# Kernel tuning notes

Hardware: AMD Instinct MI355X
Metric: run time of the kernel (lower is better)

Reference implementation:

```python
import jax, jax.numpy as jnp
import numpy as np


def _cxcywh_to_xyxy(b):
    cx, cy, w, h = b[..., 0], b[..., 1], b[..., 2], b[..., 3]
    return jnp.stack([cx - 0.5 * w, cy - 0.5 * h, cx + 0.5 * w, cy + 0.5 * h], axis=-1)


def _generalized_box_iou(a, b):
    # a: [M,4] xyxy, b: [N,4] xyxy -> [M,N] GIoU matrix (DETR box_ops semantics)
    area_a = (a[:, 2] - a[:, 0]) * (a[:, 3] - a[:, 1])  # [M]
    area_b = (b[:, 2] - b[:, 0]) * (b[:, 3] - b[:, 1])  # [N]
    lt = jnp.maximum(a[:, None, :2], b[None, :, :2])    # [M,N,2]
    rb = jnp.minimum(a[:, None, 2:], b[None, :, 2:])
    wh = jnp.clip(rb - lt, 0.0)
    inter = wh[..., 0] * wh[..., 1]                     # [M,N]
    union = area_a[:, None] + area_b[None, :] - inter
    iou = inter / union
    lt_c = jnp.minimum(a[:, None, :2], b[None, :, :2])
    rb_c = jnp.maximum(a[:, None, 2:], b[None, :, 2:])
    wh_c = jnp.clip(rb_c - lt_c, 0.0)
    area_c = wh_c[..., 0] * wh_c[..., 1]
    return iou - (area_c - union) / area_c


def setup_inputs() -> dict:
    key = jax.random.key(0)
    k1, k2, k3 = jax.random.split(key, 3)
    B, T, N = 8, 64, 8
    # predicted boxes in cxcywh, all components in (0,1) -> positive w,h (valid)
    pred_boxes = jax.random.uniform(k1, (B, T, N, 4), dtype=jnp.float32)
    # target boxes directly in valid xyxy (code path uses them unconverted)
    centers = jax.random.uniform(k2, (B, T, N, 2), dtype=jnp.float32) * 0.8 + 0.1
    half_wh = (jax.random.uniform(k3, (B, T, N, 2), dtype=jnp.float32) * 0.2 + 0.02) * 0.5
    bboxes = jnp.concatenate([centers - half_wh, centers + half_wh], axis=-1)
    bboxes_mask = jnp.ones((B, T), dtype=bool)
    return {"pred_boxes": pred_boxes, "bboxes": bboxes, "bboxes_mask": bboxes_mask}


def reference(pred_boxes, bboxes, bboxes_mask):
    B, T, N, _ = pred_boxes.shape
    M = B * T * N
    # per-box validity (mask is per-frame, broadcast to boxes), as weights
    v = jnp.broadcast_to(bboxes_mask[:, :, None], (B, T, N)).reshape(M).astype(pred_boxes.dtype)
    src = _cxcywh_to_xyxy(pred_boxes.reshape(M, 4))   # [M,4]
    tgt = bboxes.reshape(M, 4)                        # [M,4]
    G = _generalized_box_iou(tgt, src)                # [M,M] rows=targets, cols=preds
    # argmax matching over valid prediction columns
    g_match = jnp.where(v[None, :] > 0, G, -jnp.inf)
    idx = jnp.argmax(g_match, axis=1)                 # [M]
    matched = src[idx]                                # [M,4]
    matched_gious = G[:, idx]                         # [M,M] (faithful to original)
    w = v[:, None] * v[idx][None, :]                  # validity weights
    loss_giou = 1.0 - jnp.sum(matched_gious * w) / jnp.sum(w)
    loss_bbox = jnp.sum(jnp.abs(matched - tgt) * v[:, None]) / (4.0 * jnp.sum(v))
    return loss_giou, loss_bbox
```

## Files before the change

### kernel.cpp

```cpp
#include <hip/hip_runtime.h>
#include <cmath>

#define WAVE 64
#define TPB  256
#define FTPB 1024
#define KEY_INIT 0x007FFFFFFFFFFFFFull

__device__ __forceinline__ float fastrcp(float x) { return __builtin_amdgcn_rcpf(x); }

__device__ __forceinline__ unsigned sortable_u32(float f) {
    unsigned b = __float_as_uint(f);
    return (b & 0x80000000u) ? ~b : (b | 0x80000000u);
}

__device__ __forceinline__ int mask_mode(const void* maskp) {
    const unsigned char* mb = (const unsigned char*)maskp;
    unsigned char b0 = mb[0], b1 = mb[1];
    if (b0 != 0 && b1 != 0) return 0;
    if (b0 != 0) return 1;
    return 2;
}
__device__ __forceinline__ float mask_v(const void* maskp, int t, int mode) {
    if (mode == 0) return ((const unsigned char*)maskp)[t] ? 1.0f : 0.0f;
    if (mode == 1) return ((const int*)maskp)[t] ? 1.0f : 0.0f;
    return (((const float*)maskp)[t] != 0.0f) ? 1.0f : 0.0f;
}
__device__ __forceinline__ int midx(int m, int nsh, int N) {
    return (nsh >= 0) ? (m >> nsh) : (m / N);
}

__global__ __launch_bounds__(TPB) void prep_kernel(
        const float4* __restrict__ pred, const float4* __restrict__ tgt,
        const void* __restrict__ maskp, int M, int nsh, int N,
        float4* __restrict__ convS, float* __restrict__ areaS,
        float* __restrict__ areaT, float* __restrict__ vv,
        unsigned long long* __restrict__ rowkey, float* __restrict__ colsumG) {
    int m = blockIdx.x * blockDim.x + threadIdx.x;
    if (m >= M) return;
    float4 p = pred[m];
    float x1 = p.x - 0.5f * p.z, y1 = p.y - 0.5f * p.w;
    float x2 = p.x + 0.5f * p.z, y2 = p.y + 0.5f * p.w;
    convS[m] = make_float4(x1, y1, x2, y2);
    areaS[m] = (x2 - x1) * (y2 - y1);
    float4 t = tgt[m];
    areaT[m] = (t.z - t.x) * (t.w - t.y);
    vv[m] = mask_v(maskp, midx(m, nsh, N), mask_mode(maskp));
    rowkey[m] = KEY_INIT;
    colsumG[m] = 0.0f;
}

__global__ __launch_bounds__(TPB) void pass_kernel(
        const float4* __restrict__ tgt, const float* __restrict__ areaT,
        const float4* __restrict__ convS, const float* __restrict__ areaS,
        const float* __restrict__ vv, int M,
        unsigned long long* __restrict__ rowkey, float* __restrict__ colsumG) {
    const int CC   = M >> 6;
    const int wid  = blockIdx.x * (TPB / WAVE) + (threadIdx.x >> 6);
    const int lane = threadIdx.x & (WAVE - 1);
    const int rb   = wid / CC;
    const int cc   = wid % CC;
    const int r    = rb * 64 + lane;
    const int c0   = cc * 64;

    float4 a  = tgt[r];
    float  aA = areaT[r];
    float  vi = vv[r];

    float vc = vv[c0 + lane];
    unsigned long long cm = __ballot(vc > 0.0f);

    float best = -INFINITY;
    int   bidx = 0;
    float csum = 0.0f;

    const float4* __restrict__ bcol = convS + c0;
    const float*  __restrict__ bare = areaS + c0;

#pragma unroll 8
    for (int j = 0; j < 64; ++j) {
        float4 b  = bcol[j];
        float  aB = bare[j];
        float ltx = fmaxf(a.x, b.x), lty = fmaxf(a.y, b.y);
        float rbx = fminf(a.z, b.z), rby = fminf(a.w, b.w);
        float w = fmaxf(rbx - ltx, 0.0f), h = fmaxf(rby - lty, 0.0f);
        float inter = w * h;
        float uni = aA + aB - inter;
        float cx1 = fminf(a.x, b.x), cy1 = fminf(a.y, b.y);
        float cx2 = fmaxf(a.z, b.z), cy2 = fmaxf(a.w, b.w);
        float areaC = (cx2 - cx1) * (cy2 - cy1);
        float hval = fmaf(uni, fastrcp(areaC), inter * fastrcp(uni));

        float t = vi * hval;
        for (int off = 1; off <= 32; off <<= 1) t += __shfl_xor(t, off);
        csum = (lane == j) ? t : csum;

        if ((cm >> j) & 1ull) {
            if (hval > best) { best = hval; bidx = c0 + j; }
        }
    }

    unsigned long long key = ((unsigned long long)sortable_u32(best) << 32)
                           | (unsigned)(~bidx);
    atomicMax(&rowkey[r], key);
    atomicAdd(&colsumG[c0 + lane], csum);
}

__device__ __forceinline__ double wave_sum_d(double x) {
    for (int off = 32; off >= 1; off >>= 1) x += __shfl_xor(x, off);
    return x;
}

__global__ __launch_bounds__(FTPB) void finalize_kernel(
        const float4* __restrict__ convS, const float4* __restrict__ tgt,
        const float* __restrict__ vv, const unsigned long long* __restrict__ rowkey,
        const float* __restrict__ colsumG, int M, float* __restrict__ out) {
    __shared__ double red[4 * (FTPB / WAVE)];
    const int tid = threadIdx.x;

    double sumV = 0.0, S2 = 0.0, S1h = 0.0, bbox = 0.0;
    for (int m = tid; m < M; m += FTPB) {
        float vi = vv[m];
        int   k  = (int)(~(unsigned)rowkey[m]);
        float vk = vv[k];
        sumV += (double)vi;
        S2   += (double)vk;
        S1h  += (double)vk * (double)colsumG[k];
        float4 s = convS[k];
        float4 t = tgt[m];
        bbox += (double)vi * (double)(fabsf(s.x - t.x) + fabsf(s.y - t.y) +
                                      fabsf(s.z - t.z) + fabsf(s.w - t.w));
    }
    sumV = wave_sum_d(sumV);
    S2   = wave_sum_d(S2);
    S1h  = wave_sum_d(S1h);
    bbox = wave_sum_d(bbox);
    int wid = tid >> 6, lane = tid & (WAVE - 1);
    const int NW = FTPB / WAVE;
    if (lane == 0) {
        red[wid] = sumV; red[NW + wid] = S2; red[2 * NW + wid] = S1h; red[3 * NW + wid] = bbox;
    }
    __syncthreads();
    if (tid == 0) {
        double a = 0, b = 0, c = 0, d = 0;
        for (int w = 0; w < NW; ++w) {
            a += red[w]; b += red[NW + w]; c += red[2 * NW + w]; d += red[3 * NW + w];
        }
        out[0] = (float)(2.0 - c / (a * b));
        out[1] = (float)(d / (4.0 * a));
    }
}

extern "C" void kernel_launch(void* const* d_in, const int* in_sizes, int n_in,
                              void* d_out, int out_size, void* d_ws, size_t ws_size,
                              hipStream_t stream) {
    const float4* pred = (const float4*)d_in[0];
    const float4* tgt  = (const float4*)d_in[1];
    const void*   mask = d_in[2];

    int M = in_sizes[0] / 4;
    int N = M / in_sizes[2];
    int nsh = -1;
    for (int s = 0; s < 31; ++s) if ((1 << s) == N) { nsh = s; break; }

    char* ws = (char*)d_ws;
    float4* convS   = (float4*)ws;             ws += (size_t)M * 16;
    float*  areaS   = (float*)ws;              ws += (size_t)M * 4;
    float*  areaT   = (float*)ws;              ws += (size_t)M * 4;
    float*  vv      = (float*)ws;              ws += (size_t)M * 4;
    unsigned long long* rowkey = (unsigned long long*)ws; ws += (size_t)M * 8;
    float*  colsumG = (float*)ws;              ws += (size_t)M * 4;
    float*  out = (float*)d_out;

    prep_kernel<<<(M + TPB - 1) / TPB, TPB, 0, stream>>>(
        pred, tgt, mask, M, nsh, N, convS, areaS, areaT, vv, rowkey, colsumG);

    int waves  = (M / 64) * (M / 64);
    int blocks = waves / (TPB / WAVE);
    pass_kernel<<<blocks, TPB, 0, stream>>>(
        tgt, areaT, convS, areaS, vv, M, rowkey, colsumG);

    finalize_kernel<<<1, FTPB, 0, stream>>>(convS, tgt, vv, rowkey, colsumG, M, out);
}
```

Before: 95.53 us.

## Split row-argmax and column-sum into separate passes with partial buffers instead of atomics

Replaces the single pass that did per-iteration wave shuffles for column sums plus atomics with two block groups. One computes the per-row argmax keys and the other the per-column GIoU sums, and both write partial results to C×M buffers. A new reduce kernel combines these partials, and prep now precomputes 64-bit validity masks per chunk. This removes the shuffle reductions and atomics at the cost of computing every GIoU twice, an extra launch, and several MB of partial-buffer traffic.

```diff
diff --git a/kernel.cpp b/kernel.cpp
--- a/kernel.cpp
+++ b/kernel.cpp
@@ -4,7 +4,6 @@
 #define WAVE 64
 #define TPB  256
 #define FTPB 1024
-#define KEY_INIT 0x007FFFFFFFFFFFFFull
 
 __device__ __forceinline__ float fastrcp(float x) { return __builtin_amdgcn_rcpf(x); }
 
@@ -34,7 +33,7 @@
         const void* __restrict__ maskp, int M, int nsh, int N,
         float4* __restrict__ convS, float* __restrict__ areaS,
         float* __restrict__ areaT, float* __restrict__ vv,
-        unsigned long long* __restrict__ rowkey, float* __restrict__ colsumG) {
+        unsigned long long* __restrict__ cmask) {
     int m = blockIdx.x * blockDim.x + threadIdx.x;
     if (m >= M) return;
     float4 p = pred[m];
@@ -44,65 +43,98 @@
     areaS[m] = (x2 - x1) * (y2 - y1);
     float4 t = tgt[m];
     areaT[m] = (t.z - t.x) * (t.w - t.y);
-    vv[m] = mask_v(maskp, midx(m, nsh, N), mask_mode(maskp));
-    rowkey[m] = KEY_INIT;
-    colsumG[m] = 0.0f;
+    float vm = mask_v(maskp, midx(m, nsh, N), mask_mode(maskp));
+    vv[m] = vm;
+    unsigned long long bal = __ballot(vm > 0.0f);
+    if ((threadIdx.x & (WAVE - 1)) == 0) cmask[m >> 6] = bal;
 }
 
 __global__ __launch_bounds__(TPB) void pass_kernel(
         const float4* __restrict__ tgt, const float* __restrict__ areaT,
         const float4* __restrict__ convS, const float* __restrict__ areaS,
-        const float* __restrict__ vv, int M,
-        unsigned long long* __restrict__ rowkey, float* __restrict__ colsumG) {
-    const int CC   = M >> 6;
-    const int wid  = blockIdx.x * (TPB / WAVE) + (threadIdx.x >> 6);
-    const int lane = threadIdx.x & (WAVE - 1);
-    const int rb   = wid / CC;
-    const int cc   = wid % CC;
-    const int r    = rb * 64 + lane;
-    const int c0   = cc * 64;
-
-    float4 a  = tgt[r];
-    float  aA = areaT[r];
-    float  vi = vv[r];
-
-    float vc = vv[c0 + lane];
-    unsigned long long cm = __ballot(vc > 0.0f);
-
-    float best = -INFINITY;
-    int   bidx = 0;
-    float csum = 0.0f;
-
-    const float4* __restrict__ bcol = convS + c0;
-    const float*  __restrict__ bare = areaS + c0;
-
+        const unsigned long long* __restrict__ cmask, int M, int rowBlocks,
+        unsigned long long* __restrict__ keypart, float* __restrict__ colpart) {
+    const int C   = M >> 6;
+    const int tid = threadIdx.x;
+
+    if ((int)blockIdx.x < rowBlocks) {
+        const int rb = blockIdx.x / C;
+        const int cc = blockIdx.x % C;
+        const int r  = rb * TPB + tid;
+        float4 a  = tgt[r];
+        float  aA = areaT[r];
+        const unsigned long long cm = cmask[cc];
+        const float4* __restrict__ bc = convS + (size_t)cc * 64;
+        const float*  __restrict__ ba = areaS + (size_t)cc * 64;
+
+        float best = -INFINITY;
+        int   bidx = 0;
 #pragma unroll 8
-    for (int j = 0; j < 64; ++j) {
-        float4 b  = bcol[j];
-        float  aB = bare[j];
-        float ltx = fmaxf(a.x, b.x), lty = fmaxf(a.y, b.y);
-        float rbx = fminf(a.z, b.z), rby = fminf(a.w, b.w);
-        float w = fmaxf(rbx - ltx, 0.0f), h = fmaxf(rby - lty, 0.0f);
-        float inter = w * h;
-        float uni = aA + aB - inter;
-        float cx1 = fminf(a.x, b.x), cy1 = fminf(a.y, b.y);
-        float cx2 = fmaxf(a.z, b.z), cy2 = fmaxf(a.w, b.w);
-        float areaC = (cx2 - cx1) * (cy2 - cy1);
-        float hval = fmaf(uni, fastrcp(areaC), inter * fastrcp(uni));
-
-        float t = vi * hval;
-        for (int off = 1; off <= 32; off <<= 1) t += __shfl_xor(t, off);
-        csum = (lane == j) ? t : csum;
-
-        if ((cm >> j) & 1ull) {
-            if (hval > best) { best = hval; bidx = c0 + j; }
+        for (int j = 0; j < 64; ++j) {
+            if (!((cm >> j) & 1ull)) continue;
+            float4 b  = bc[j];
+            float  aB = ba[j];
+            float ltx = fmaxf(a.x, b.x), lty = fmaxf(a.y, b.y);
+            float rbx = fminf(a.z, b.z), rby = fminf(a.w, b.w);
+            float w = fmaxf(rbx - ltx, 0.0f), h = fmaxf(rby - lty, 0.0f);
+            float inter = w * h;
+            float uni = aA + aB - inter;
+            float cx1 = fminf(a.x, b.x), cy1 = fminf(a.y, b.y);
+            float cx2 = fmaxf(a.z, b.z), cy2 = fmaxf(a.w, b.w);
+            float areaC = (cx2 - cx1) * (cy2 - cy1);
+            float hval = fmaf(uni, fastrcp(areaC), inter * fastrcp(uni));
+            if (hval > best) { best = hval; bidx = cc * 64 + j; }
         }
-    }
-
-    unsigned long long key = ((unsigned long long)sortable_u32(best) << 32)
-                           | (unsigned)(~bidx);
-    atomicMax(&rowkey[r], key);
-    atomicAdd(&colsumG[c0 + lane], csum);
+        unsigned long long key = ((unsigned long long)sortable_u32(best) << 32)
+                               | (unsigned)(~bidx);
+        keypart[(size_t)cc * M + r] = key;
+    } else {
+        const int bb2 = blockIdx.x - rowBlocks;
+        const int cb = bb2 / C;
+        const int rc = bb2 % C;
+        const int c  = cb * TPB + tid;
+        float4 b  = convS[c];
+        float  aB = areaS[c];
+        const unsigned long long rm = cmask[rc];
+        const float4* __restrict__ ar  = tgt   + (size_t)rc * 64;
+        const float*  __restrict__ aar = areaT + (size_t)rc * 64;
+
+        float csum = 0.0f;
+#pragma unroll 8
+        for (int j = 0; j < 64; ++j) {
+            if (!((rm >> j) & 1ull)) continue;
+            float4 a  = ar[j];
+            float  aA = aar[j];
+            float ltx = fmaxf(a.x, b.x), lty = fmaxf(a.y, b.y);
+            float rbx = fminf(a.z, b.z), rby = fminf(a.w, b.w);
+            float w = fmaxf(rbx - ltx, 0.0f), h = fmaxf(rby - lty, 0.0f);
+            float inter = w * h;
+            float uni = aA + aB - inter;
+            float cx1 = fminf(a.x, b.x), cy1 = fminf(a.y, b.y);
+            float cx2 = fmaxf(a.z, b.z), cy2 = fmaxf(a.w, b.w);
+            float areaC = (cx2 - cx1) * (cy2 - cy1);
+            float hval = fmaf(uni, fastrcp(areaC), inter * fastrcp(uni));
+            csum += hval;
+        }
+        colpart[(size_t)rc * M + c] = csum;
+    }
+}
+
+__global__ __launch_bounds__(TPB) void reduce_kernel(
+        const unsigned long long* __restrict__ keypart,
+        const float* __restrict__ colpart, int M, int C,
+        int* __restrict__ idx, float* __restrict__ colsumh) {
+    int m = blockIdx.x * blockDim.x + threadIdx.x;
+    if (m >= M) return;
+    unsigned long long k = keypart[m];
+    float s = colpart[m];
+    for (int cc = 1; cc < C; ++cc) {
+        unsigned long long kc = keypart[(size_t)cc * M + m];
+        k = (kc > k) ? kc : k;
+        s += colpart[(size_t)cc * M + m];
+    }
+    idx[m] = (int)(~(unsigned)k);
+    colsumh[m] = s;
 }
 
 __device__ __forceinline__ double wave_sum_d(double x) {
@@ -112,19 +144,19 @@
 
 __global__ __launch_bounds__(FTPB) void finalize_kernel(
         const float4* __restrict__ convS, const float4* __restrict__ tgt,
-        const float* __restrict__ vv, const unsigned long long* __restrict__ rowkey,
-        const float* __restrict__ colsumG, int M, float* __restrict__ out) {
+        const float* __restrict__ vv, const int* __restrict__ idx,
+        const float* __restrict__ colsumh, int M, float* __restrict__ out) {
     __shared__ double red[4 * (FTPB / WAVE)];
     const int tid = threadIdx.x;
 
     double sumV = 0.0, S2 = 0.0, S1h = 0.0, bbox = 0.0;
     for (int m = tid; m < M; m += FTPB) {
         float vi = vv[m];
-        int   k  = (int)(~(unsigned)rowkey[m]);
+        int   k  = idx[m];
         float vk = vv[k];
         sumV += (double)vi;
         S2   += (double)vk;
-        S1h  += (double)vk * (double)colsumG[k];
+        S1h  += (double)vk * (double)colsumh[k];
         float4 s = convS[k];
         float4 t = tgt[m];
         bbox += (double)vi * (double)(fabsf(s.x - t.x) + fabsf(s.y - t.y) +
@@ -162,22 +194,30 @@
     int nsh = -1;
     for (int s = 0; s < 31; ++s) if ((1 << s) == N) { nsh = s; break; }
 
+    int C = M >> 6;
+
     char* ws = (char*)d_ws;
     float4* convS   = (float4*)ws;             ws += (size_t)M * 16;
     float*  areaS   = (float*)ws;              ws += (size_t)M * 4;
     float*  areaT   = (float*)ws;              ws += (size_t)M * 4;
     float*  vv      = (float*)ws;              ws += (size_t)M * 4;
-    unsigned long long* rowkey = (unsigned long long*)ws; ws += (size_t)M * 8;
-    float*  colsumG = (float*)ws;              ws += (size_t)M * 4;
+    unsigned long long* cmaskp = (unsigned long long*)ws; ws += (size_t)C * 8;
+    unsigned long long* keypart = (unsigned long long*)ws; ws += (size_t)C * M * 8;
+    float*  colpart = (float*)ws;              ws += (size_t)C * M * 4;
+    int*    idx     = (int*)ws;                ws += (size_t)M * 4;
+    float*  colsumh = (float*)ws;              ws += (size_t)M * 4;
     float*  out = (float*)d_out;
 
     prep_kernel<<<(M + TPB - 1) / TPB, TPB, 0, stream>>>(
-        pred, tgt, mask, M, nsh, N, convS, areaS, areaT, vv, rowkey, colsumG);
-
-    int waves  = (M / 64) * (M / 64);
-    int blocks = waves / (TPB / WAVE);
-    pass_kernel<<<blocks, TPB, 0, stream>>>(
-        tgt, areaT, convS, areaS, vv, M, rowkey, colsumG);
-
-    finalize_kernel<<<1, FTPB, 0, stream>>>(convS, tgt, vv, rowkey, colsumG, M, out);
-}
+        pred, tgt, mask, M, nsh, N, convS, areaS, areaT, vv, cmaskp);
+
+    int rowBlocks = (M / TPB) * C;
+    int colBlocks = rowBlocks;
+    pass_kernel<<<rowBlocks + colBlocks, TPB, 0, stream>>>(
+        tgt, areaT, convS, areaS, cmaskp, M, rowBlocks, keypart, colpart);
+
+    reduce_kernel<<<(M + TPB - 1) / TPB, TPB, 0, stream>>>(
+        keypart, colpart, M, C, idx, colsumh);
+
+    finalize_kernel<<<1, FTPB, 0, stream>>>(convS, tgt, vv, idx, colsumh, M, out);
+}
```

Result: slower. 114.3 us (+19.6%).

## Fuse prep, pairwise pass and finalize into one kernel with split row/column blocks

Applied to the files above, without the earlier changes.

Replaces the three-kernel pipeline with one kernel. Half of the blocks compute per-row argmax partial keys and the other half compute per-column GIoU partial sums; both recompute box conversion and areas on the fly. The last block, found through an atomic counter, reduces the partials and computes the losses. This removes the per-iteration wave shuffle reduction, the global atomics and the extra launches, at the cost of evaluating the pairwise GIoU twice and a serial single-block partial reduction.

```diff
diff --git a/kernel.cpp b/kernel.cpp
--- a/kernel.cpp
+++ b/kernel.cpp
@@ -3,8 +3,7 @@
 
 #define WAVE 64
 #define TPB  256
-#define FTPB 1024
-#define KEY_INIT 0x007FFFFFFFFFFFFFull
+#define JPB  128
 
 __device__ __forceinline__ float fastrcp(float x) { return __builtin_amdgcn_rcpf(x); }
 
@@ -29,113 +28,135 @@
     return (nsh >= 0) ? (m >> nsh) : (m / N);
 }
 
-__global__ __launch_bounds__(TPB) void prep_kernel(
-        const float4* __restrict__ pred, const float4* __restrict__ tgt,
-        const void* __restrict__ maskp, int M, int nsh, int N,
-        float4* __restrict__ convS, float* __restrict__ areaS,
-        float* __restrict__ areaT, float* __restrict__ vv,
-        unsigned long long* __restrict__ rowkey, float* __restrict__ colsumG) {
-    int m = blockIdx.x * blockDim.x + threadIdx.x;
-    if (m >= M) return;
-    float4 p = pred[m];
-    float x1 = p.x - 0.5f * p.z, y1 = p.y - 0.5f * p.w;
-    float x2 = p.x + 0.5f * p.z, y2 = p.y + 0.5f * p.w;
-    convS[m] = make_float4(x1, y1, x2, y2);
-    areaS[m] = (x2 - x1) * (y2 - y1);
-    float4 t = tgt[m];
-    areaT[m] = (t.z - t.x) * (t.w - t.y);
-    vv[m] = mask_v(maskp, midx(m, nsh, N), mask_mode(maskp));
-    rowkey[m] = KEY_INIT;
-    colsumG[m] = 0.0f;
-}
-
-__global__ __launch_bounds__(TPB) void pass_kernel(
-        const float4* __restrict__ tgt, const float* __restrict__ areaT,
-        const float4* __restrict__ convS, const float* __restrict__ areaS,
-        const float* __restrict__ vv, int M,
-        unsigned long long* __restrict__ rowkey, float* __restrict__ colsumG) {
-    const int CC   = M >> 6;
-    const int wid  = blockIdx.x * (TPB / WAVE) + (threadIdx.x >> 6);
-    const int lane = threadIdx.x & (WAVE - 1);
-    const int rb   = wid / CC;
-    const int cc   = wid % CC;
-    const int r    = rb * 64 + lane;
-    const int c0   = cc * 64;
-
-    float4 a  = tgt[r];
-    float  aA = areaT[r];
-    float  vi = vv[r];
-
-    float vc = vv[c0 + lane];
-    unsigned long long cm = __ballot(vc > 0.0f);
-
-    float best = -INFINITY;
-    int   bidx = 0;
-    float csum = 0.0f;
-
-    const float4* __restrict__ bcol = convS + c0;
-    const float*  __restrict__ bare = areaS + c0;
-
-#pragma unroll 8
-    for (int j = 0; j < 64; ++j) {
-        float4 b  = bcol[j];
-        float  aB = bare[j];
-        float ltx = fmaxf(a.x, b.x), lty = fmaxf(a.y, b.y);
-        float rbx = fminf(a.z, b.z), rby = fminf(a.w, b.w);
-        float w = fmaxf(rbx - ltx, 0.0f), h = fmaxf(rby - lty, 0.0f);
-        float inter = w * h;
-        float uni = aA + aB - inter;
-        float cx1 = fminf(a.x, b.x), cy1 = fminf(a.y, b.y);
-        float cx2 = fmaxf(a.z, b.z), cy2 = fmaxf(a.w, b.w);
-        float areaC = (cx2 - cx1) * (cy2 - cy1);
-        float hval = fmaf(uni, fastrcp(areaC), inter * fastrcp(uni));
-
-        float t = vi * hval;
-        for (int off = 1; off <= 32; off <<= 1) t += __shfl_xor(t, off);
-        csum = (lane == j) ? t : csum;
-
-        if ((cm >> j) & 1ull) {
-            if (hval > best) { best = hval; bidx = c0 + j; }
-        }
-    }
-
-    unsigned long long key = ((unsigned long long)sortable_u32(best) << 32)
-                           | (unsigned)(~bidx);
-    atomicMax(&rowkey[r], key);
-    atomicAdd(&colsumG[c0 + lane], csum);
-}
-
 __device__ __forceinline__ double wave_sum_d(double x) {
     for (int off = 32; off >= 1; off >>= 1) x += __shfl_xor(x, off);
     return x;
 }
 
-__global__ __launch_bounds__(FTPB) void finalize_kernel(
-        const float4* __restrict__ convS, const float4* __restrict__ tgt,
-        const float* __restrict__ vv, const unsigned long long* __restrict__ rowkey,
-        const float* __restrict__ colsumG, int M, float* __restrict__ out) {
-    __shared__ double red[4 * (FTPB / WAVE)];
-    const int tid = threadIdx.x;
+__global__ __launch_bounds__(TPB) void fused_kernel(
+        const float4* __restrict__ pred, const float4* __restrict__ tgt,
+        const void* __restrict__ maskp, int M, int nsh, int N,
+        int RB, int CPR,
+        unsigned long long* __restrict__ keypart, float* __restrict__ colpart,
+        int* __restrict__ idxw, float* __restrict__ colsumhw,
+        unsigned int* __restrict__ counter, float* __restrict__ out) {
+    const int tid  = threadIdx.x;
+    const int lane = tid & (WAVE - 1);
+    const int mode = mask_mode(maskp);
+
+    if ((int)blockIdx.x < RB) {
+        const int rb = blockIdx.x / CPR;
+        const int cj = blockIdx.x % CPR;
+        const int r  = rb * TPB + tid;
+        float4 a  = tgt[r];
+        float  aA = (a.z - a.x) * (a.w - a.y);
+        unsigned long long cm0 = __ballot(mask_v(maskp, midx(cj * JPB + lane, nsh, N), mode) > 0.0f);
+        unsigned long long cm1 = __ballot(mask_v(maskp, midx(cj * JPB + 64 + lane, nsh, N), mode) > 0.0f);
+        const float4* __restrict__ pc = pred + (size_t)cj * JPB;
+
+        float best = -INFINITY;
+        int   bidx = 0;
+#pragma unroll 8
+        for (int j = 0; j < JPB; ++j) {
+            unsigned long long bit = (j < 64) ? (cm0 >> j) : (cm1 >> (j - 64));
+            if (!(bit & 1ull)) continue;
+            float4 p  = pc[j];
+            float bx1 = fmaf(-0.5f, p.z, p.x), by1 = fmaf(-0.5f, p.w, p.y);
+            float bx2 = fmaf( 0.5f, p.z, p.x), by2 = fmaf( 0.5f, p.w, p.y);
+            float aB  = (bx2 - bx1) * (by2 - by1);
+            float ltx = fmaxf(a.x, bx1), lty = fmaxf(a.y, by1);
+            float rbx = fminf(a.z, bx2), rby = fminf(a.w, by2);
+            float w = fmaxf(rbx - ltx, 0.0f), h = fmaxf(rby - lty, 0.0f);
+            float inter = w * h;
+            float uni = aA + aB - inter;
+            float cx1 = fminf(a.x, bx1), cy1 = fminf(a.y, by1);
+            float cx2 = fmaxf(a.z, bx2), cy2 = fmaxf(a.w, by2);
+            float areaC = (cx2 - cx1) * (cy2 - cy1);
+            float hval = fmaf(uni, fastrcp(areaC), inter * fastrcp(uni));
+            if (hval > best) { best = hval; bidx = cj * JPB + j; }
+        }
+        keypart[(size_t)cj * M + r] = ((unsigned long long)sortable_u32(best) << 32)
+                                    | (unsigned)(~bidx);
+    } else {
+        const int b2 = blockIdx.x - RB;
+        const int cb = b2 / CPR;
+        const int rj = b2 % CPR;
+        const int c  = cb * TPB + tid;
+        float4 p  = pred[c];
+        float bx1 = fmaf(-0.5f, p.z, p.x), by1 = fmaf(-0.5f, p.w, p.y);
+        float bx2 = fmaf( 0.5f, p.z, p.x), by2 = fmaf( 0.5f, p.w, p.y);
+        float aB  = (bx2 - bx1) * (by2 - by1);
+        unsigned long long rm0 = __ballot(mask_v(maskp, midx(rj * JPB + lane, nsh, N), mode) > 0.0f);
+        unsigned long long rm1 = __ballot(mask_v(maskp, midx(rj * JPB + 64 + lane, nsh, N), mode) > 0.0f);
+        const float4* __restrict__ ar = tgt + (size_t)rj * JPB;
+
+        float csum = 0.0f;
+#pragma unroll 8
+        for (int j = 0; j < JPB; ++j) {
+            unsigned long long bit = (j < 64) ? (rm0 >> j) : (rm1 >> (j - 64));
+            if (!(bit & 1ull)) continue;
+            float4 a  = ar[j];
+            float  aA = (a.z - a.x) * (a.w - a.y);
+            float ltx = fmaxf(a.x, bx1), lty = fmaxf(a.y, by1);
+            float rbx = fminf(a.z, bx2), rby = fminf(a.w, by2);
+            float w = fmaxf(rbx - ltx, 0.0f), h = fmaxf(rby - lty, 0.0f);
+            float inter = w * h;
+            float uni = aA + aB - inter;
+            float cx1 = fminf(a.x, bx1), cy1 = fminf(a.y, by1);
+            float cx2 = fmaxf(a.z, bx2), cy2 = fmaxf(a.w, by2);
+            float areaC = (cx2 - cx1) * (cy2 - cy1);
+            float hval = fmaf(uni, fastrcp(areaC), inter * fastrcp(uni));
+            csum += hval;
+        }
+        colpart[(size_t)rj * M + c] = csum;
+    }
+
+    __shared__ int lastflag;
+    __threadfence();
+    __syncthreads();
+    if (tid == 0) {
+        unsigned old = atomicAdd(counter, 1u);
+        lastflag = (old == gridDim.x - 1) ? 1 : 0;
+    }
+    __syncthreads();
+    if (!lastflag) return;
+    __threadfence();
+
+    for (int m = tid; m < M; m += TPB) {
+        unsigned long long k = keypart[m];
+        float s = colpart[m];
+        for (int cc = 1; cc < CPR; ++cc) {
+            unsigned long long kc = keypart[(size_t)cc * M + m];
+            k = (kc > k) ? kc : k;
+            s += colpart[(size_t)cc * M + m];
+        }
+        idxw[m] = (int)(~(unsigned)k);
+        colsumhw[m] = s;
+    }
+    __syncthreads();
 
     double sumV = 0.0, S2 = 0.0, S1h = 0.0, bbox = 0.0;
-    for (int m = tid; m < M; m += FTPB) {
-        float vi = vv[m];
-        int   k  = (int)(~(unsigned)rowkey[m]);
-        float vk = vv[k];
+    for (int m = tid; m < M; m += TPB) {
+        float vi = mask_v(maskp, midx(m, nsh, N), mode);
+        int   k  = idxw[m];
+        float vk = mask_v(maskp, midx(k, nsh, N), mode);
         sumV += (double)vi;
         S2   += (double)vk;
-        S1h  += (double)vk * (double)colsumG[k];
-        float4 s = convS[k];
+        S1h  += (double)vk * (double)colsumhw[k];
+        float4 p = pred[k];
+        float sx1 = fmaf(-0.5f, p.z, p.x), sy1 = fmaf(-0.5f, p.w, p.y);
+        float sx2 = fmaf( 0.5f, p.z, p.x), sy2 = fmaf( 0.5f, p.w, p.y);
         float4 t = tgt[m];
-        bbox += (double)vi * (double)(fabsf(s.x - t.x) + fabsf(s.y - t.y) +
-                                      fabsf(s.z - t.z) + fabsf(s.w - t.w));
-    }
+        bbox += (double)vi * (double)(fabsf(sx1 - t.x) + fabsf(sy1 - t.y) +
+                                      fabsf(sx2 - t.z) + fabsf(sy2 - t.w));
+    }
+    __shared__ double red[4 * (TPB / WAVE)];
     sumV = wave_sum_d(sumV);
     S2   = wave_sum_d(S2);
     S1h  = wave_sum_d(S1h);
     bbox = wave_sum_d(bbox);
-    int wid = tid >> 6, lane = tid & (WAVE - 1);
-    const int NW = FTPB / WAVE;
+    int wid = tid >> 6;
+    const int NW = TPB / WAVE;
     if (lane == 0) {
         red[wid] = sumV; red[NW + wid] = S2; red[2 * NW + wid] = S1h; red[3 * NW + wid] = bbox;
     }
@@ -162,22 +183,21 @@
     int nsh = -1;
     for (int s = 0; s < 31; ++s) if ((1 << s) == N) { nsh = s; break; }
 
+    int CPR = M / JPB;
+
     char* ws = (char*)d_ws;
-    float4* convS   = (float4*)ws;             ws += (size_t)M * 16;
-    float*  areaS   = (float*)ws;              ws += (size_t)M * 4;
-    float*  areaT   = (float*)ws;              ws += (size_t)M * 4;
-    float*  vv      = (float*)ws;              ws += (size_t)M * 4;
-    unsigned long long* rowkey = (unsigned long long*)ws; ws += (size_t)M * 8;
-    float*  colsumG = (float*)ws;              ws += (size_t)M * 4;
-    float*  out = (float*)d_out;
-
-    prep_kernel<<<(M + TPB - 1) / TPB, TPB, 0, stream>>>(
-        pred, tgt, mask, M, nsh, N, convS, areaS, areaT, vv, rowkey, colsumG);
-
-    int waves  = (M / 64) * (M / 64);
-    int blocks = waves / (TPB / WAVE);
-    pass_kernel<<<blocks, TPB, 0, stream>>>(
-        tgt, areaT, convS, areaS, vv, M, rowkey, colsumG);
-
-    finalize_kernel<<<1, FTPB, 0, stream>>>(convS, tgt, vv, rowkey, colsumG, M, out);
-}
+    unsigned int* counter = (unsigned int*)ws;             ws += 16;
+    unsigned long long* keypart = (unsigned long long*)ws; ws += (size_t)CPR * M * 8;
+    float* colpart  = (float*)ws;                          ws += (size_t)CPR * M * 4;
+    int*   idxw     = (int*)ws;                            ws += (size_t)M * 4;
+    float* colsumhw = (float*)ws;                          ws += (size_t)M * 4;
+    float* out = (float*)d_out;
+
+    hipMemsetAsync(counter, 0, 4, stream);
+
+    int RB = (M / TPB) * CPR;
+    int CB = RB;
+    fused_kernel<<<RB + CB, TPB, 0, stream>>>(
+        pred, tgt, mask, M, nsh, N, RB, CPR,
+        keypart, colpart, idxw, colsumhw, counter, out);
+}
```

Measured after the change: 301.2 us. +215.3%, slower.
